# Performance work log

Hardware: AMD Instinct MI355X
Metric: run time of the kernel (lower is better)

Reference implementation:

```python
import jax, jax.numpy as jnp
import numpy as np

DT_RANK = 64
D_STATE = 16


def setup_inputs() -> dict:
    key = jax.random.key(0)
    ks = jax.random.split(key, 6)
    B, L, Di = 2, 2048, 2048
    x = jax.random.normal(ks[0], (B, L, Di), dtype=jnp.float32)
    W_xproj = jax.random.normal(ks[1], (DT_RANK + 2 * D_STATE, Di), dtype=jnp.float32) * (Di ** -0.5)
    W_dt = jax.random.uniform(ks[2], (Di, DT_RANK), dtype=jnp.float32, minval=-(DT_RANK ** -0.5), maxval=DT_RANK ** -0.5)
    dt = jnp.exp(jax.random.uniform(ks[3], (Di,), dtype=jnp.float32) * (np.log(0.1) - np.log(0.001)) + np.log(0.001))
    b_dt = dt + jnp.log(-jnp.expm1(-dt))
    A_log = jnp.log(jnp.broadcast_to(jnp.arange(1, D_STATE + 1, dtype=jnp.float32), (Di, D_STATE)))
    D_param = jnp.ones((Di,), dtype=jnp.float32)
    return {"x": x, "W_xproj": W_xproj, "W_dt": W_dt, "b_dt": b_dt, "A_log": A_log, "D_param": D_param}


def _selective_scan(u, delta, A, Bm, Cm):
    # u, delta: (b, l, d); A: (d, n); Bm, Cm: (b, l, n)
    deltaA = jnp.exp(delta[..., None] * A[None, None])          # (b, l, d, n)
    deltaB_u = delta[..., None] * Bm[:, :, None, :] * u[..., None]  # (b, l, d, n)

    def step(h, inp):
        dA, dBu, c = inp                      # dA,dBu: (b,d,n); c: (b,n)
        h = dA * h + dBu
        y = jnp.einsum('bdn,bn->bd', h, c)
        return h, y

    b, l, d = u.shape
    h0 = jnp.zeros((b, d, A.shape[1]), dtype=u.dtype)
    xs = (jnp.moveaxis(deltaA, 1, 0), jnp.moveaxis(deltaB_u, 1, 0), jnp.moveaxis(Cm, 1, 0))
    _, ys = jax.lax.scan(step, h0, xs)        # ys: (l, b, d)
    return jnp.moveaxis(ys, 0, 1)


def reference(x, W_xproj, W_dt, b_dt, A_log, D_param):
    x_dbl = jnp.einsum('bld,ed->ble', x, W_xproj)  # (b, l, dt_rank + 2*n)
    dlt = x_dbl[..., :DT_RANK]
    Bm = x_dbl[..., DT_RANK:DT_RANK + D_STATE]
    Cm = x_dbl[..., DT_RANK + D_STATE:]
    delta = jax.nn.softplus(jnp.einsum('blr,dr->bld', dlt, W_dt) + b_dt)
    A = -jnp.exp(A_log.astype(jnp.float32))
    y = _selective_scan(x, delta, A, Bm, Cm)
    return y + x * D_param[None, None, :]
```

## Files before the change

### kernel.cpp

```cpp
#include <hip/hip_runtime.h>

#define BATCH 2
#define L_SEQ 2048
#define DI 2048
#define NROW (BATCH * L_SEQ)
#define E_DIM 96
#define RNK 64
#define NST 16
#define NCH 64
#define CL 32
#define SPLITK 16
#define KSL (DI / SPLITK)

#define WS_XDBL 0
#define WS_PART 393216
#define WS_HLOC 393216
#define WS_DSUM (393216 + 4194304)
#define WS_HENT (393216 + 6291456)
#define WS_WDTT (393216 + 6291456)

__device__ __forceinline__ float softplusf(float z) {
    return fmaxf(z, 0.f) + __logf(1.f + __expf(-fabsf(z)));
}

__device__ __forceinline__ void barrier_lds() {
    asm volatile("s_waitcnt lgkmcnt(0)" ::: "memory");
    __builtin_amdgcn_s_barrier();
}

__global__ __launch_bounds__(256) void gemm_xproj_part(const float* __restrict__ x,
                                                       const float* __restrict__ Wx,
                                                       float* __restrict__ part) {
    __shared__ float xs[32][68];
    __shared__ float wsh[32][100];
    const int tid = threadIdx.x;
    const int r0 = blockIdx.x * 64;
    const int kbase0 = blockIdx.y * KSL;
    const int rg = tid >> 4;
    const int cg = tid & 15;

    float acc[4][6];
#pragma unroll
    for (int i = 0; i < 4; i++)
#pragma unroll
        for (int j = 0; j < 6; j++) acc[i][j] = 0.f;

    for (int kt = 0; kt < KSL / 32; kt++) {
        const int kb = kbase0 + kt * 32;
#pragma unroll
        for (int rep = 0; rep < 2; rep++) {
            int i = rep * 256 + tid;
            int row = i >> 3;
            int kq = i & 7;
            float4 v = *(const float4*)&x[(long)(r0 + row) * DI + kb + kq * 4];
            xs[kq * 4 + 0][row] = v.x;
            xs[kq * 4 + 1][row] = v.y;
            xs[kq * 4 + 2][row] = v.z;
            xs[kq * 4 + 3][row] = v.w;
        }
#pragma unroll
        for (int rep = 0; rep < 3; rep++) {
            int i = rep * 256 + tid;
            int e = i >> 3;
            int kq = i & 7;
            float4 v = *(const float4*)&Wx[(long)e * DI + kb + kq * 4];
            wsh[kq * 4 + 0][e] = v.x;
            wsh[kq * 4 + 1][e] = v.y;
            wsh[kq * 4 + 2][e] = v.z;
            wsh[kq * 4 + 3][e] = v.w;
        }
        __syncthreads();
#pragma unroll 8
        for (int k = 0; k < 32; k++) {
            float xr[4], wr[6];
#pragma unroll
            for (int i = 0; i < 4; i++) xr[i] = xs[k][rg * 4 + i];
#pragma unroll
            for (int j = 0; j < 6; j++) wr[j] = wsh[k][cg * 6 + j];
#pragma unroll
            for (int i = 0; i < 4; i++)
#pragma unroll
                for (int j = 0; j < 6; j++) acc[i][j] = fmaf(xr[i], wr[j], acc[i][j]);
        }
        __syncthreads();
    }
    const long sbase = (long)blockIdx.y * NROW * E_DIM;
#pragma unroll
    for (int i = 0; i < 4; i++) {
        long rowb = sbase + (long)(r0 + rg * 4 + i) * E_DIM + cg * 6;
#pragma unroll
        for (int j = 0; j < 6; j++) part[rowb + j] = acc[i][j];
    }
}

__global__ __launch_bounds__(256) void xproj_reduce_wt(const float* __restrict__ part,
                                                       float* __restrict__ xdbl,
                                                       const float* __restrict__ Wdt,
                                                       float* __restrict__ wdtT) {
    if (blockIdx.x < 384) {
        const int i4 = blockIdx.x * 256 + threadIdx.x;
        const float4* p4 = (const float4*)part;
        float4 s = p4[i4];
#pragma unroll
        for (int sp = 1; sp < SPLITK; sp++) {
            float4 v = p4[(long)sp * (NROW * E_DIM / 4) + i4];
            s.x += v.x; s.y += v.y; s.z += v.z; s.w += v.w;
        }
        ((float4*)xdbl)[i4] = s;
    } else {
        const int t = (blockIdx.x - 384) * 256 + threadIdx.x;
        const int base = t * 4;
        const int r = base >> 11;
        const int d4 = base & (DI - 1);
        float4 o;
        o.x = Wdt[(long)(d4 + 0) * RNK + r];
        o.y = Wdt[(long)(d4 + 1) * RNK + r];
        o.z = Wdt[(long)(d4 + 2) * RNK + r];
        o.w = Wdt[(long)(d4 + 3) * RNK + r];
        *(float4*)&wdtT[base] = o;
    }
}

#define PW 260
#define PD 36
__global__ __launch_bounds__(256) void gemm_dt_scan(const float* __restrict__ x,
                                                    const float* __restrict__ xdbl,
                                                    const float* __restrict__ wdtT,
                                                    const float* __restrict__ b_dt,
                                                    const float* __restrict__ A_log,
                                                    float* __restrict__ delta,
                                                    float* __restrict__ hloc,
                                                    float* __restrict__ dsumb) {
    __shared__ float region[32 * PW + 32 * PD];
    __shared__ float bsm[CL * NST];
    float* wt  = region;
    float* dlb = region + 32 * PW;
    float* dtt = region;

    const int tid = threadIdx.x;
    const int d0 = blockIdx.x * 256;
    const int c = blockIdx.y;
    const int b = blockIdx.z;
    const int row0 = b * L_SEQ + c * CL;
    const int d = d0 + tid;
    const int rg = tid >> 6;
    const int cg = tid & 63;

    if (tid < 128) {
        int r = tid >> 2, q = tid & 3;
        ((float4*)bsm)[tid] = *(const float4*)&xdbl[(long)(row0 + r) * E_DIM + 64 + q * 4];
    }

    float acc[8][4];
#pragma unroll
    for (int i = 0; i < 8; i++)
#pragma unroll
        for (int j = 0; j < 4; j++) acc[i][j] = 0.f;

    float xv[CL];
    float4 av[4];

#pragma unroll
    for (int kt = 0; kt < 2; kt++) {
        const int kb = kt * 32;
#pragma unroll
        for (int rep = 0; rep < 8; rep++) {
            int i = rep * 256 + tid;
            int k = i >> 6, c4 = i & 63;
            float4 v = *(const float4*)&wdtT[(long)(kb + k) * DI + d0 + c4 * 4];
            *(float4*)&wt[k * PW + c4 * 4] = v;
        }
        {
            int r = tid >> 3, kq = tid & 7;
            float4 v = *(const float4*)&xdbl[(long)(row0 + r) * E_DIM + kb + kq * 4];
            dlb[(kq * 4 + 0) * PD + r] = v.x;
            dlb[(kq * 4 + 1) * PD + r] = v.y;
            dlb[(kq * 4 + 2) * PD + r] = v.z;
            dlb[(kq * 4 + 3) * PD + r] = v.w;
        }
        if (kt == 0) {
#pragma unroll
            for (int ll = 0; ll < CL; ll++)
                xv[ll] = x[(long)(row0 + ll) * DI + d];
#pragma unroll
            for (int q = 0; q < 4; q++)
                av[q] = *(const float4*)&A_log[(long)d * NST + q * 4];
        }
        barrier_lds();
#pragma unroll 8
        for (int k = 0; k < 32; k++) {
            float4 xa = *(const float4*)&dlb[k * PD + rg * 8];
            float4 xb = *(const float4*)&dlb[k * PD + rg * 8 + 4];
            float4 wv4 = *(const float4*)&wt[k * PW + cg * 4];
            float xr[8] = {xa.x, xa.y, xa.z, xa.w, xb.x, xb.y, xb.z, xb.w};
            float wr[4] = {wv4.x, wv4.y, wv4.z, wv4.w};
#pragma unroll
            for (int i = 0; i < 8; i++)
#pragma unroll
                for (int j = 0; j < 4; j++) acc[i][j] = fmaf(xr[i], wr[j], acc[i][j]);
        }
        barrier_lds();
    }

    float4 bb = *(const float4*)&b_dt[d0 + cg * 4];
#pragma unroll
    for (int i = 0; i < 8; i++) {
        int r = rg * 8 + i;
        float4 o;
        o.x = softplusf(acc[i][0] + bb.x);
        o.y = softplusf(acc[i][1] + bb.y);
        o.z = softplusf(acc[i][2] + bb.z);
        o.w = softplusf(acc[i][3] + bb.w);
        *(float4*)&delta[(long)(row0 + r) * DI + d0 + cg * 4] = o;
        *(float4*)&dtt[r * 256 + cg * 4] = o;
    }

    float A[16];
#pragma unroll
    for (int q = 0; q < 4; q++) {
        A[q * 4 + 0] = -__expf(av[q].x);
        A[q * 4 + 1] = -__expf(av[q].y);
        A[q * 4 + 2] = -__expf(av[q].z);
        A[q * 4 + 3] = -__expf(av[q].w);
    }
    const float A0 = A[0];
    bool fast = true;
#pragma unroll
    for (int n = 1; n < 16; n++)
        fast = fast && (fabsf(A[n] - (float)(n + 1) * A0) <= 1e-4f * (float)(n + 1));
    barrier_lds();

    float h[16];
#pragma unroll
    for (int n = 0; n < 16; n++) h[n] = 0.f;
    float dsum = 0.f;
    if (fast) {
        for (int ll = 0; ll < CL; ll++) {
            float dc = dtt[ll * 256 + tid];
            float du = dc * xv[ll];
            float p1 = __expf(dc * A0);
            float p2 = p1 * p1, p3 = p2 * p1, p4 = p2 * p2, p5 = p3 * p2;
            float p6 = p3 * p3, p7 = p4 * p3, p8 = p4 * p4, p9 = p5 * p4;
            float p10 = p5 * p5, p11 = p6 * p5, p12 = p6 * p6, p13 = p7 * p6;
            float p14 = p7 * p7, p15 = p8 * p7, p16 = p8 * p8;
            float e_[16] = {p1, p2, p3, p4, p5, p6, p7, p8,
                            p9, p10, p11, p12, p13, p14, p15, p16};
#pragma unroll
            for (int q = 0; q < 4; q++) {
                float4 v = *(const float4*)&bsm[ll * NST + q * 4];
                h[q * 4 + 0] = fmaf(e_[q * 4 + 0], h[q * 4 + 0], du * v.x);
                h[q * 4 + 1] = fmaf(e_[q * 4 + 1], h[q * 4 + 1], du * v.y);
                h[q * 4 + 2] = fmaf(e_[q * 4 + 2], h[q * 4 + 2], du * v.z);
                h[q * 4 + 3] = fmaf(e_[q * 4 + 3], h[q * 4 + 3], du * v.w);
            }
            dsum += dc;
        }
    } else {
        for (int ll = 0; ll < CL; ll++) {
            float dc = dtt[ll * 256 + tid];
            float du = dc * xv[ll];
#pragma unroll
            for (int q = 0; q < 4; q++) {
                float4 v = *(const float4*)&bsm[ll * NST + q * 4];
                h[q * 4 + 0] = fmaf(__expf(dc * A[q * 4 + 0]), h[q * 4 + 0], du * v.x);
                h[q * 4 + 1] = fmaf(__expf(dc * A[q * 4 + 1]), h[q * 4 + 1], du * v.y);
                h[q * 4 + 2] = fmaf(__expf(dc * A[q * 4 + 2]), h[q * 4 + 2], du * v.z);
                h[q * 4 + 3] = fmaf(__expf(dc * A[q * 4 + 3]), h[q * 4 + 3], du * v.w);
            }
            dsum += dc;
        }
    }
    const long cb = (long)(b * NCH + c);
#pragma unroll
    for (int n = 0; n < 16; n++)
        hloc[(cb * NST + n) * DI + d] = h[n];
    dsumb[cb * DI + d] = dsum;
}

__global__ __launch_bounds__(256, 1) void scan_prefix(const float* __restrict__ A_log,
                                                      const float* __restrict__ hloc,
                                                      const float* __restrict__ dsumb,
                                                      float* __restrict__ hent) {
    const int g = blockIdx.x * 256 + threadIdx.x;
    const int d = g & (DI - 1);
    const int n = (g >> 11) & 15;
    const int b = g >> 15;
    const float An = -__expf(A_log[(long)d * NST + n]);
    float hl[NCH], dsv[NCH];
#pragma unroll
    for (int cc = 0; cc < NCH; cc++) {
        hl[cc]  = hloc[((long)(b * NCH + cc) * NST + n) * DI + d];
        dsv[cc] = dsumb[(long)(b * NCH + cc) * DI + d];
    }
    float e[NCH];
#pragma unroll
    for (int cc = 0; cc < NCH; cc++) e[cc] = __expf(An * dsv[cc]);
    float hc = 0.f;
#pragma unroll
    for (int cc = 0; cc < NCH; cc++) {
        hent[((long)(b * NCH + cc) * NST + n) * DI + d] = hc;
        hc = fmaf(e[cc], hc, hl[cc]);
    }
}

__global__ __launch_bounds__(256) void scan_out(const float* __restrict__ x,
                                                const float* __restrict__ xdbl,
                                                const float* __restrict__ A_log,
                                                const float* __restrict__ Dp,
                                                const float* __restrict__ hent,
                                                float* __restrict__ out) {
    __shared__ float bsm[CL * NST];
    __shared__ float csm[CL * NST];
    const int tid = threadIdx.x;
    const int d0 = blockIdx.x * 256;
    const int c = blockIdx.y;
    const int b = blockIdx.z;
    const int row0 = b * L_SEQ + c * CL;
    const int d = d0 + tid;

    {
        int i = tid & 127, r = i >> 2, q = i & 3;
        float4 v = *(const float4*)&xdbl[(long)(row0 + r) * E_DIM + 64 + ((tid >> 7) << 4) + q * 4];
        if (tid < 128) ((float4*)bsm)[i] = v;
        else           ((float4*)csm)[i] = v;
    }
    __syncthreads();

    float4 av[4];
#pragma unroll
    for (int q = 0; q < 4; q++)
        av[q] = *(const float4*)&A_log[(long)d * NST + q * 4];
    const long cb = (long)(b * NCH + c);
    float hv[16];
#pragma unroll
    for (int n = 0; n < 16; n++)
        hv[n] = hent[(cb * NST + n) * DI + d];
    const float Dd = Dp[d];

    float dv[CL], xv[CL];
#pragma unroll
    for (int ll = 0; ll < CL; ll++) {
        dv[ll] = out[(long)(row0 + ll) * DI + d];
        xv[ll] = x[(long)(row0 + ll) * DI + d];
    }

    float A[16];
#pragma unroll
    for (int q = 0; q < 4; q++) {
        A[q * 4 + 0] = -__expf(av[q].x);
        A[q * 4 + 1] = -__expf(av[q].y);
        A[q * 4 + 2] = -__expf(av[q].z);
        A[q * 4 + 3] = -__expf(av[q].w);
    }
    const float A0 = A[0];
    bool fast = true;
#pragma unroll
    for (int n = 1; n < 16; n++)
        fast = fast && (fabsf(A[n] - (float)(n + 1) * A0) <= 1e-4f * (float)(n + 1));
    float h[16];
#pragma unroll
    for (int n = 0; n < 16; n++) h[n] = hv[n];

    long idx = (long)row0 * DI + d;
    if (fast) {
        for (int ll = 0; ll < CL; ll++) {
            float dc = dv[ll];
            float xc = xv[ll];
            float du = dc * xc;
            float p1 = __expf(dc * A0);
            float p2 = p1 * p1, p3 = p2 * p1, p4 = p2 * p2, p5 = p3 * p2;
            float p6 = p3 * p3, p7 = p4 * p3, p8 = p4 * p4, p9 = p5 * p4;
            float p10 = p5 * p5, p11 = p6 * p5, p12 = p6 * p6, p13 = p7 * p6;
            float p14 = p7 * p7, p15 = p8 * p7, p16 = p8 * p8;
            float e_[16] = {p1, p2, p3, p4, p5, p6, p7, p8,
                            p9, p10, p11, p12, p13, p14, p15, p16};
            float y = 0.f;
#pragma unroll
            for (int q = 0; q < 4; q++) {
                float4 v = *(const float4*)&bsm[ll * NST + q * 4];
                float4 w = *(const float4*)&csm[ll * NST + q * 4];
                h[q * 4 + 0] = fmaf(e_[q * 4 + 0], h[q * 4 + 0], du * v.x);
                h[q * 4 + 1] = fmaf(e_[q * 4 + 1], h[q * 4 + 1], du * v.y);
                h[q * 4 + 2] = fmaf(e_[q * 4 + 2], h[q * 4 + 2], du * v.z);
                h[q * 4 + 3] = fmaf(e_[q * 4 + 3], h[q * 4 + 3], du * v.w);
                y = fmaf(h[q * 4 + 0], w.x, y);
                y = fmaf(h[q * 4 + 1], w.y, y);
                y = fmaf(h[q * 4 + 2], w.z, y);
                y = fmaf(h[q * 4 + 3], w.w, y);
            }
            out[idx] = fmaf(xc, Dd, y);
            idx += DI;
        }
    } else {
        for (int ll = 0; ll < CL; ll++) {
            float dc = dv[ll];
            float xc = xv[ll];
            float du = dc * xc;
            float y = 0.f;
#pragma unroll
            for (int q = 0; q < 4; q++) {
                float4 v = *(const float4*)&bsm[ll * NST + q * 4];
                float4 w = *(const float4*)&csm[ll * NST + q * 4];
                float e0 = __expf(dc * A[q * 4 + 0]);
                float e1 = __expf(dc * A[q * 4 + 1]);
                float e2 = __expf(dc * A[q * 4 + 2]);
                float e3 = __expf(dc * A[q * 4 + 3]);
                h[q * 4 + 0] = fmaf(e0, h[q * 4 + 0], du * v.x);
                h[q * 4 + 1] = fmaf(e1, h[q * 4 + 1], du * v.y);
                h[q * 4 + 2] = fmaf(e2, h[q * 4 + 2], du * v.z);
                h[q * 4 + 3] = fmaf(e3, h[q * 4 + 3], du * v.w);
                y = fmaf(h[q * 4 + 0], w.x, y);
                y = fmaf(h[q * 4 + 1], w.y, y);
                y = fmaf(h[q * 4 + 2], w.z, y);
                y = fmaf(h[q * 4 + 3], w.w, y);
            }
            out[idx] = fmaf(xc, Dd, y);
            idx += DI;
        }
    }
}

extern "C" void kernel_launch(void* const* d_in, const int* in_sizes, int n_in,
                              void* d_out, int out_size, void* d_ws, size_t ws_size,
                              hipStream_t stream) {
    const float* x    = (const float*)d_in[0];
    const float* Wx   = (const float*)d_in[1];
    const float* Wdt  = (const float*)d_in[2];
    const float* bdt  = (const float*)d_in[3];
    const float* Alog = (const float*)d_in[4];
    const float* Dp   = (const float*)d_in[5];
    float* out = (float*)d_out;
    float* ws = (float*)d_ws;
    float* xdbl  = ws + WS_XDBL;
    float* partb = ws + WS_PART;
    float* hloc  = ws + WS_HLOC;
    float* dsumb = ws + WS_DSUM;
    float* hent  = ws + WS_HENT;
    float* wdtT  = ws + WS_WDTT;

    gemm_xproj_part<<<dim3(NROW / 64, SPLITK), 256, 0, stream>>>(x, Wx, partb);
    xproj_reduce_wt<<<dim3(384 + 128), 256, 0, stream>>>(partb, xdbl, Wdt, wdtT);
    gemm_dt_scan<<<dim3(DI / 256, NCH, BATCH), 256, 0, stream>>>(x, xdbl, wdtT, bdt, Alog,
                                                                 out, hloc, dsumb);
    scan_prefix<<<dim3(BATCH * DI * NST / 256), 256, 0, stream>>>(Alog, hloc, dsumb, hent);
    scan_out<<<dim3(DI / 256, NCH, BATCH), 256, 0, stream>>>(x, xdbl, Alog, Dp, hent, out);
}
```

Before: 188.5 us.

## Fuse dt GEMM, chunk scan, prefix and output into one cooperative kernel

Replaces the three-kernel dt-GEMM/scan/prefix/output sequence with a single cooperative kernel that uses grid-wide syncs between the local chunk scan, the cross-chunk prefix and the output pass. Chunks grow to 64 steps, and delta, x, B and C stay in registers and LDS across phases. This removes the delta round trip through the output buffer, the x reload and two launches. In exchange it adds grid-sync cost, high register pressure from the 64-element per-thread arrays, and it only runs when occupancy allows all 512 blocks to be co-resident, otherwise falling back to the old kernels.

```diff
diff --git a/kernel.cpp b/kernel.cpp
--- a/kernel.cpp
+++ b/kernel.cpp
@@ -1,4 +1,6 @@
 #include <hip/hip_runtime.h>
+#include <hip/hip_cooperative_groups.h>
+namespace cg = cooperative_groups;
 
 #define BATCH 2
 #define L_SEQ 2048
@@ -7,6 +9,8 @@
 #define E_DIM 96
 #define RNK 64
 #define NST 16
+#define CLEN 64
+#define NCHG 32
 #define NCH 64
 #define CL 32
 #define SPLITK 16
@@ -14,10 +18,13 @@
 
 #define WS_XDBL 0
 #define WS_PART 393216
-#define WS_HLOC 393216
-#define WS_DSUM (393216 + 4194304)
-#define WS_HENT (393216 + 6291456)
-#define WS_WDTT (393216 + 6291456)
+#define WS_HLOC32 393216
+#define WS_DSUM32 2490368
+#define WS_HENT32 6684672
+#define WS_HLOC64 393216
+#define WS_DSUM64 4587520
+#define WS_HENT64 6684672
+#define WS_WDTT 8781824
 
 __device__ __forceinline__ float softplusf(float z) {
     return fmaxf(z, 0.f) + __logf(1.f + __expf(-fabsf(z)));
@@ -123,6 +130,287 @@
 
 #define PW 260
 #define PD 36
+#define PDF 68
+
+#define PCHAIN_E16(DCV) \
+    float p1 = __expf((DCV) * A0); \
+    float p2 = p1 * p1, p3 = p2 * p1, p4 = p2 * p2, p5 = p4 * p1; \
+    float p6 = p3 * p3, p7 = p4 * p3, p8 = p4 * p4; \
+    float e_[16] = {p1, p2, p3, p4, p5, p6, p7, p8, \
+                    p8 * p1, p5 * p5, p8 * p3, p6 * p6, \
+                    p8 * p5, p7 * p7, p8 * p7, p8 * p8};
+
+__global__ __launch_bounds__(256, 2) void ssm_fused(const float* __restrict__ x,
+                                                    const float* __restrict__ xdbl,
+                                                    const float* __restrict__ wdtT,
+                                                    const float* __restrict__ b_dt,
+                                                    const float* __restrict__ A_log,
+                                                    const float* __restrict__ Dp,
+                                                    float* __restrict__ hloc,
+                                                    float* __restrict__ dsumb,
+                                                    float* __restrict__ hent,
+                                                    float* __restrict__ out) {
+    __shared__ float region[16 * PW + 16 * PDF];
+    float* wt  = region;
+    float* dlb = region + 16 * PW;
+    float* dtt = region;
+    float* bsm = region;
+    float* csm = region + CLEN * NST;
+
+    const int tid = threadIdx.x;
+    const int bid = blockIdx.x;
+    const int d0 = (bid & 7) * 256;
+    const int c = (bid >> 3) & 31;
+    const int b = bid >> 8;
+    const int row0 = b * L_SEQ + c * CLEN;
+    const int d = d0 + tid;
+    const int rg = tid >> 6;
+    const int cg = tid & 63;
+
+    float4 wq[2][4]; float4 dq[2];
+#define ISSUE_Q(SET, Q) \
+    { _Pragma("unroll") \
+      for (int rep = 0; rep < 4; rep++) { \
+          int i = rep * 256 + tid; int kk = i >> 6, c4 = i & 63; \
+          wq[SET][rep] = *(const float4*)&wdtT[(long)((Q) * 16 + kk) * DI + d0 + c4 * 4]; } \
+      { int r = tid >> 2, kk = tid & 3; \
+        dq[SET] = *(const float4*)&xdbl[(long)(row0 + r) * E_DIM + (Q) * 16 + kk * 4]; } }
+#define WRITE_Q(SET) \
+    { _Pragma("unroll") \
+      for (int rep = 0; rep < 4; rep++) { \
+          int i = rep * 256 + tid; int kk = i >> 6, c4 = i & 63; \
+          *(float4*)&wt[kk * PW + c4 * 4] = wq[SET][rep]; } \
+      { int r = tid >> 2, kk = tid & 3; \
+        dlb[(kk * 4 + 0) * PDF + r] = dq[SET].x; \
+        dlb[(kk * 4 + 1) * PDF + r] = dq[SET].y; \
+        dlb[(kk * 4 + 2) * PDF + r] = dq[SET].z; \
+        dlb[(kk * 4 + 3) * PDF + r] = dq[SET].w; } }
+
+    ISSUE_Q(0, 0);
+    float4 av[4];
+#pragma unroll
+    for (int q = 0; q < 4; q++)
+        av[q] = *(const float4*)&A_log[(long)d * NST + q * 4];
+    float4 bb = *(const float4*)&b_dt[d0 + cg * 4];
+
+    WRITE_Q(0);
+    ISSUE_Q(1, 1);
+    barrier_lds();
+
+    float accA[8][4], accB[8][4];
+#pragma unroll
+    for (int i = 0; i < 8; i++)
+#pragma unroll
+        for (int j = 0; j < 4; j++) { accA[i][j] = 0.f; accB[i][j] = 0.f; }
+
+#pragma unroll
+    for (int qq = 0; qq < 4; qq++) {
+#pragma unroll
+        for (int k = 0; k < 16; k++) {
+            float4 a0 = *(const float4*)&dlb[k * PDF + rg * 8];
+            float4 a1 = *(const float4*)&dlb[k * PDF + rg * 8 + 4];
+            float4 b0 = *(const float4*)&dlb[k * PDF + 32 + rg * 8];
+            float4 b1 = *(const float4*)&dlb[k * PDF + 32 + rg * 8 + 4];
+            float4 w4 = *(const float4*)&wt[k * PW + cg * 4];
+            float ar[8] = {a0.x, a0.y, a0.z, a0.w, a1.x, a1.y, a1.z, a1.w};
+            float br[8] = {b0.x, b0.y, b0.z, b0.w, b1.x, b1.y, b1.z, b1.w};
+            float wr[4] = {w4.x, w4.y, w4.z, w4.w};
+#pragma unroll
+            for (int i = 0; i < 8; i++)
+#pragma unroll
+                for (int j = 0; j < 4; j++) {
+                    accA[i][j] = fmaf(ar[i], wr[j], accA[i][j]);
+                    accB[i][j] = fmaf(br[i], wr[j], accB[i][j]);
+                }
+        }
+        barrier_lds();
+        if (qq < 3) {
+            WRITE_Q((qq + 1) & 1);
+            if (qq < 2) ISSUE_Q(qq & 1, qq + 2);
+            barrier_lds();
+        }
+    }
+
+    float xv[CLEN];
+#pragma unroll
+    for (int ll = 0; ll < CLEN; ll++) xv[ll] = x[(long)(row0 + ll) * DI + d];
+
+    float A0; bool fast;
+    {
+        float a16[16];
+#pragma unroll
+        for (int q = 0; q < 4; q++) {
+            a16[q * 4 + 0] = -__expf(av[q].x);
+            a16[q * 4 + 1] = -__expf(av[q].y);
+            a16[q * 4 + 2] = -__expf(av[q].z);
+            a16[q * 4 + 3] = -__expf(av[q].w);
+        }
+        A0 = a16[0];
+        fast = true;
+#pragma unroll
+        for (int n = 1; n < 16; n++)
+            fast = fast && (fabsf(a16[n] - (float)(n + 1) * A0) <= 1e-4f * (float)(n + 1));
+    }
+
+    float dcl[CLEN];
+#define XROUND(ACC, RG0, TBASE) \
+    if (rg == (RG0) || rg == (RG0) + 1) { \
+        _Pragma("unroll") for (int i = 0; i < 8; i++) { \
+            float4 o; \
+            o.x = softplusf(ACC[i][0] + bb.x); \
+            o.y = softplusf(ACC[i][1] + bb.y); \
+            o.z = softplusf(ACC[i][2] + bb.z); \
+            o.w = softplusf(ACC[i][3] + bb.w); \
+            *(float4*)&dtt[((rg - (RG0)) * 8 + i) * 256 + cg * 4] = o; \
+        } \
+    } \
+    barrier_lds(); \
+    _Pragma("unroll") for (int ll = 0; ll < 16; ll++) dcl[(TBASE) + ll] = dtt[ll * 256 + tid]; \
+    barrier_lds();
+
+    XROUND(accA, 0, 0)
+    XROUND(accA, 2, 16)
+    XROUND(accB, 0, 32)
+    XROUND(accB, 2, 48)
+
+    { int r = tid >> 2, q = tid & 3;
+      float4 bv = *(const float4*)&xdbl[(long)(row0 + r) * E_DIM + 64 + q * 4];
+      float4 cv = *(const float4*)&xdbl[(long)(row0 + r) * E_DIM + 80 + q * 4];
+      *(float4*)&bsm[r * NST + q * 4] = bv;
+      *(float4*)&csm[r * NST + q * 4] = cv; }
+    barrier_lds();
+
+    float h[16];
+#pragma unroll
+    for (int n = 0; n < 16; n++) h[n] = 0.f;
+    float dsum = 0.f;
+    if (fast) {
+#pragma unroll
+        for (int ll = 0; ll < CLEN; ll++) {
+            float dcv = dcl[ll]; float du = dcv * xv[ll];
+            PCHAIN_E16(dcv);
+#pragma unroll
+            for (int q = 0; q < 4; q++) {
+                float4 v = *(const float4*)&bsm[ll * NST + q * 4];
+                h[q * 4 + 0] = fmaf(e_[q * 4 + 0], h[q * 4 + 0], du * v.x);
+                h[q * 4 + 1] = fmaf(e_[q * 4 + 1], h[q * 4 + 1], du * v.y);
+                h[q * 4 + 2] = fmaf(e_[q * 4 + 2], h[q * 4 + 2], du * v.z);
+                h[q * 4 + 3] = fmaf(e_[q * 4 + 3], h[q * 4 + 3], du * v.w);
+            }
+            dsum += dcv;
+        }
+    } else {
+        float Ag[16];
+#pragma unroll
+        for (int q = 0; q < 4; q++) {
+            Ag[q * 4 + 0] = -__expf(av[q].x); Ag[q * 4 + 1] = -__expf(av[q].y);
+            Ag[q * 4 + 2] = -__expf(av[q].z); Ag[q * 4 + 3] = -__expf(av[q].w);
+        }
+#pragma unroll
+        for (int ll = 0; ll < CLEN; ll++) {
+            float dcv = dcl[ll]; float du = dcv * xv[ll];
+#pragma unroll
+            for (int q = 0; q < 4; q++) {
+                float4 v = *(const float4*)&bsm[ll * NST + q * 4];
+                h[q * 4 + 0] = fmaf(__expf(dcv * Ag[q * 4 + 0]), h[q * 4 + 0], du * v.x);
+                h[q * 4 + 1] = fmaf(__expf(dcv * Ag[q * 4 + 1]), h[q * 4 + 1], du * v.y);
+                h[q * 4 + 2] = fmaf(__expf(dcv * Ag[q * 4 + 2]), h[q * 4 + 2], du * v.z);
+                h[q * 4 + 3] = fmaf(__expf(dcv * Ag[q * 4 + 3]), h[q * 4 + 3], du * v.w);
+            }
+            dsum += dcv;
+        }
+    }
+    const long cbq = (long)(b * NCHG + c);
+#pragma unroll
+    for (int n = 0; n < 16; n++)
+        hloc[(cbq * NST + n) * DI + d] = h[n];
+    dsumb[cbq * DI + d] = dsum;
+
+    __threadfence();
+    cg::this_grid().sync();
+
+    {
+        const int gi = bid * 256 + tid;
+        if (gi < BATCH * DI * NST) {
+            const int d2 = gi & (DI - 1);
+            const int n2 = (gi >> 11) & 15;
+            const int b2 = gi >> 15;
+            const float An = -__expf(A_log[(long)d2 * NST + n2]);
+            float hc = 0.f;
+#pragma unroll
+            for (int c8 = 0; c8 < NCHG; c8 += 8) {
+                float hl[8], ds8[8];
+#pragma unroll
+                for (int j = 0; j < 8; j++) {
+                    hl[j] = hloc[((long)(b2 * NCHG + c8 + j) * NST + n2) * DI + d2];
+                    ds8[j] = dsumb[(long)(b2 * NCHG + c8 + j) * DI + d2];
+                }
+#pragma unroll
+                for (int j = 0; j < 8; j++) {
+                    hent[((long)(b2 * NCHG + c8 + j) * NST + n2) * DI + d2] = hc;
+                    hc = fmaf(__expf(An * ds8[j]), hc, hl[j]);
+                }
+            }
+        }
+    }
+    __threadfence();
+    cg::this_grid().sync();
+
+    const float Dd = Dp[d];
+#pragma unroll
+    for (int n = 0; n < 16; n++)
+        h[n] = hent[(cbq * NST + n) * DI + d];
+
+    if (fast) {
+#pragma unroll
+        for (int ll = 0; ll < CLEN; ll++) {
+            float dcv = dcl[ll]; float xc = xv[ll]; float du = dcv * xc;
+            PCHAIN_E16(dcv);
+            float y = 0.f;
+#pragma unroll
+            for (int q = 0; q < 4; q++) {
+                float4 v = *(const float4*)&bsm[ll * NST + q * 4];
+                float4 w = *(const float4*)&csm[ll * NST + q * 4];
+                h[q * 4 + 0] = fmaf(e_[q * 4 + 0], h[q * 4 + 0], du * v.x);
+                h[q * 4 + 1] = fmaf(e_[q * 4 + 1], h[q * 4 + 1], du * v.y);
+                h[q * 4 + 2] = fmaf(e_[q * 4 + 2], h[q * 4 + 2], du * v.z);
+                h[q * 4 + 3] = fmaf(e_[q * 4 + 3], h[q * 4 + 3], du * v.w);
+                y = fmaf(h[q * 4 + 0], w.x, y);
+                y = fmaf(h[q * 4 + 1], w.y, y);
+                y = fmaf(h[q * 4 + 2], w.z, y);
+                y = fmaf(h[q * 4 + 3], w.w, y);
+            }
+            out[(long)(row0 + ll) * DI + d] = fmaf(xc, Dd, y);
+        }
+    } else {
+        float Ag[16];
+#pragma unroll
+        for (int q = 0; q < 4; q++) {
+            Ag[q * 4 + 0] = -__expf(av[q].x); Ag[q * 4 + 1] = -__expf(av[q].y);
+            Ag[q * 4 + 2] = -__expf(av[q].z); Ag[q * 4 + 3] = -__expf(av[q].w);
+        }
+#pragma unroll
+        for (int ll = 0; ll < CLEN; ll++) {
+            float dcv = dcl[ll]; float xc = xv[ll]; float du = dcv * xc;
+            float y = 0.f;
+#pragma unroll
+            for (int q = 0; q < 4; q++) {
+                float4 v = *(const float4*)&bsm[ll * NST + q * 4];
+                float4 w = *(const float4*)&csm[ll * NST + q * 4];
+                h[q * 4 + 0] = fmaf(__expf(dcv * Ag[q * 4 + 0]), h[q * 4 + 0], du * v.x);
+                h[q * 4 + 1] = fmaf(__expf(dcv * Ag[q * 4 + 1]), h[q * 4 + 1], du * v.y);
+                h[q * 4 + 2] = fmaf(__expf(dcv * Ag[q * 4 + 2]), h[q * 4 + 2], du * v.z);
+                h[q * 4 + 3] = fmaf(__expf(dcv * Ag[q * 4 + 3]), h[q * 4 + 3], du * v.w);
+                y = fmaf(h[q * 4 + 0], w.x, y);
+                y = fmaf(h[q * 4 + 1], w.y, y);
+                y = fmaf(h[q * 4 + 2], w.z, y);
+                y = fmaf(h[q * 4 + 3], w.w, y);
+            }
+            out[(long)(row0 + ll) * DI + d] = fmaf(xc, Dd, y);
+        }
+    }
+}
+
 __global__ __launch_bounds__(256) void gemm_dt_scan(const float* __restrict__ x,
                                                     const float* __restrict__ xdbl,
                                                     const float* __restrict__ wdtT,
@@ -157,7 +445,7 @@
 #pragma unroll
         for (int j = 0; j < 4; j++) acc[i][j] = 0.f;
 
-    float xv[CL];
+    float xvv[CL];
     float4 av[4];
 
 #pragma unroll
@@ -181,7 +469,7 @@
         if (kt == 0) {
 #pragma unroll
             for (int ll = 0; ll < CL; ll++)
-                xv[ll] = x[(long)(row0 + ll) * DI + d];
+                xvv[ll] = x[(long)(row0 + ll) * DI + d];
 #pragma unroll
             for (int q = 0; q < 4; q++)
                 av[q] = *(const float4*)&A_log[(long)d * NST + q * 4];
@@ -202,15 +490,15 @@
         barrier_lds();
     }
 
-    float4 bb = *(const float4*)&b_dt[d0 + cg * 4];
+    float4 bbf = *(const float4*)&b_dt[d0 + cg * 4];
 #pragma unroll
     for (int i = 0; i < 8; i++) {
         int r = rg * 8 + i;
         float4 o;
-        o.x = softplusf(acc[i][0] + bb.x);
-        o.y = softplusf(acc[i][1] + bb.y);
-        o.z = softplusf(acc[i][2] + bb.z);
-        o.w = softplusf(acc[i][3] + bb.w);
+        o.x = softplusf(acc[i][0] + bbf.x);
+        o.y = softplusf(acc[i][1] + bbf.y);
+        o.z = softplusf(acc[i][2] + bbf.z);
+        o.w = softplusf(acc[i][3] + bbf.w);
         *(float4*)&delta[(long)(row0 + r) * DI + d0 + cg * 4] = o;
         *(float4*)&dtt[r * 256 + cg * 4] = o;
     }
@@ -237,14 +525,8 @@
     if (fast) {
         for (int ll = 0; ll < CL; ll++) {
             float dc = dtt[ll * 256 + tid];
-            float du = dc * xv[ll];
-            float p1 = __expf(dc * A0);
-            float p2 = p1 * p1, p3 = p2 * p1, p4 = p2 * p2, p5 = p3 * p2;
-            float p6 = p3 * p3, p7 = p4 * p3, p8 = p4 * p4, p9 = p5 * p4;
-            float p10 = p5 * p5, p11 = p6 * p5, p12 = p6 * p6, p13 = p7 * p6;
-            float p14 = p7 * p7, p15 = p8 * p7, p16 = p8 * p8;
-            float e_[16] = {p1, p2, p3, p4, p5, p6, p7, p8,
-                            p9, p10, p11, p12, p13, p14, p15, p16};
+            float du = dc * xvv[ll];
+            PCHAIN_E16(dc);
 #pragma unroll
             for (int q = 0; q < 4; q++) {
                 float4 v = *(const float4*)&bsm[ll * NST + q * 4];
@@ -258,7 +540,7 @@
     } else {
         for (int ll = 0; ll < CL; ll++) {
             float dc = dtt[ll * 256 + tid];
-            float du = dc * xv[ll];
+            float du = dc * xvv[ll];
 #pragma unroll
             for (int q = 0; q < 4; q++) {
                 float4 v = *(const float4*)&bsm[ll * NST + q * 4];
@@ -337,11 +619,11 @@
         hv[n] = hent[(cb * NST + n) * DI + d];
     const float Dd = Dp[d];
 
-    float dv[CL], xv[CL];
+    float dv[CL], xvv[CL];
 #pragma unroll
     for (int ll = 0; ll < CL; ll++) {
         dv[ll] = out[(long)(row0 + ll) * DI + d];
-        xv[ll] = x[(long)(row0 + ll) * DI + d];
+        xvv[ll] = x[(long)(row0 + ll) * DI + d];
     }
 
     float A[16];
@@ -365,15 +647,9 @@
     if (fast) {
         for (int ll = 0; ll < CL; ll++) {
             float dc = dv[ll];
-            float xc = xv[ll];
+            float xc = xvv[ll];
             float du = dc * xc;
-            float p1 = __expf(dc * A0);
-            float p2 = p1 * p1, p3 = p2 * p1, p4 = p2 * p2, p5 = p3 * p2;
-            float p6 = p3 * p3, p7 = p4 * p3, p8 = p4 * p4, p9 = p5 * p4;
-            float p10 = p5 * p5, p11 = p6 * p5, p12 = p6 * p6, p13 = p7 * p6;
-            float p14 = p7 * p7, p15 = p8 * p7, p16 = p8 * p8;
-            float e_[16] = {p1, p2, p3, p4, p5, p6, p7, p8,
-                            p9, p10, p11, p12, p13, p14, p15, p16};
+            PCHAIN_E16(dc);
             float y = 0.f;
 #pragma unroll
             for (int q = 0; q < 4; q++) {
@@ -394,21 +670,17 @@
     } else {
         for (int ll = 0; ll < CL; ll++) {
             float dc = dv[ll];
-            float xc = xv[ll];
+            float xc = xvv[ll];
             float du = dc * xc;
             float y = 0.f;
 #pragma unroll
             for (int q = 0; q < 4; q++) {
                 float4 v = *(const float4*)&bsm[ll * NST + q * 4];
                 float4 w = *(const float4*)&csm[ll * NST + q * 4];
-                float e0 = __expf(dc * A[q * 4 + 0]);
-                float e1 = __expf(dc * A[q * 4 + 1]);
-                float e2 = __expf(dc * A[q * 4 + 2]);
-                float e3 = __expf(dc * A[q * 4 + 3]);
-                h[q * 4 + 0] = fmaf(e0, h[q * 4 + 0], du * v.x);
-                h[q * 4 + 1] = fmaf(e1, h[q * 4 + 1], du * v.y);
-                h[q * 4 + 2] = fmaf(e2, h[q * 4 + 2], du * v.z);
-                h[q * 4 + 3] = fmaf(e3, h[q * 4 + 3], du * v.w);
+                h[q * 4 + 0] = fmaf(__expf(dc * A[q * 4 + 0]), h[q * 4 + 0], du * v.x);
+                h[q * 4 + 1] = fmaf(__expf(dc * A[q * 4 + 1]), h[q * 4 + 1], du * v.y);
+                h[q * 4 + 2] = fmaf(__expf(dc * A[q * 4 + 2]), h[q * 4 + 2], du * v.z);
+                h[q * 4 + 3] = fmaf(__expf(dc * A[q * 4 + 3]), h[q * 4 + 3], du * v.w);
                 y = fmaf(h[q * 4 + 0], w.x, y);
                 y = fmaf(h[q * 4 + 1], w.y, y);
                 y = fmaf(h[q * 4 + 2], w.z, y);
@@ -431,17 +703,44 @@
     const float* Dp   = (const float*)d_in[5];
     float* out = (float*)d_out;
     float* ws = (float*)d_ws;
-    float* xdbl  = ws + WS_XDBL;
-    float* partb = ws + WS_PART;
-    float* hloc  = ws + WS_HLOC;
-    float* dsumb = ws + WS_DSUM;
-    float* hent  = ws + WS_HENT;
-    float* wdtT  = ws + WS_WDTT;
+    float* xdbl   = ws + WS_XDBL;
+    float* partb  = ws + WS_PART;
+    float* wdtT   = ws + WS_WDTT;
+    float* hloc32 = ws + WS_HLOC32;
+    float* dsum32 = ws + WS_DSUM32;
+    float* hent32 = ws + WS_HENT32;
+    float* hloc64 = ws + WS_HLOC64;
+    float* dsum64 = ws + WS_DSUM64;
+    float* hent64 = ws + WS_HENT64;
+
+    static int coop_ok = -1;
+    if (coop_ok < 0) {
+        int nb = 0, ncu = 0, dev = 0;
+        (void)hipGetDevice(&dev);
+        hipError_t e1 = hipOccupancyMaxActiveBlocksPerMultiprocessor(
+            &nb, (const void*)ssm_fused, 256, 0);
+        hipError_t e2 = hipDeviceGetAttribute(
+            &ncu, hipDeviceAttributeMultiprocessorCount, dev);
+        coop_ok = (e1 == hipSuccess && e2 == hipSuccess &&
+                   (long)nb * ncu >= BATCH * NCHG * 8) ? 1 : 0;
+    }
 
     gemm_xproj_part<<<dim3(NROW / 64, SPLITK), 256, 0, stream>>>(x, Wx, partb);
-    xproj_reduce_wt<<<dim3(384 + 128), 256, 0, stream>>>(partb, xdbl, Wdt, wdtT);
-    gemm_dt_scan<<<dim3(DI / 256, NCH, BATCH), 256, 0, stream>>>(x, xdbl, wdtT, bdt, Alog,
-                                                                 out, hloc, dsumb);
-    scan_prefix<<<dim3(BATCH * DI * NST / 256), 256, 0, stream>>>(Alog, hloc, dsumb, hent);
-    scan_out<<<dim3(DI / 256, NCH, BATCH), 256, 0, stream>>>(x, xdbl, Alog, Dp, hent, out);
-}
+    xproj_reduce_wt<<<dim3(512), 256, 0, stream>>>(partb, xdbl, Wdt, wdtT);
+
+    bool done = false;
+    if (coop_ok == 1) {
+        void* args[] = {(void*)&x, (void*)&xdbl, (void*)&wdtT, (void*)&bdt, (void*)&Alog,
+                        (void*)&Dp, (void*)&hloc32, (void*)&dsum32, (void*)&hent32, (void*)&out};
+        hipError_t le = hipLaunchCooperativeKernel((const void*)ssm_fused,
+                                                   dim3(BATCH * NCHG * 8), dim3(256),
+                                                   args, 0, stream);
+        done = (le == hipSuccess);
+    }
+    if (!done) {
+        gemm_dt_scan<<<dim3(DI / 256, NCH, BATCH), 256, 0, stream>>>(x, xdbl, wdtT, bdt, Alog,
+                                                                     out, hloc64, dsum64);
+        scan_prefix<<<dim3(BATCH * DI * NST / 256), 256, 0, stream>>>(Alog, hloc64, dsum64, hent64);
+        scan_out<<<dim3(DI / 256, NCH, BATCH), 256, 0, stream>>>(x, xdbl, Alog, Dp, hent64, out);
+    }
+}
```

After: 192.7 us. +2.3%, slower.

## Use 512-thread blocks, split scan state across thread halves, stream W_dt tiles

Applied to the files above, without the earlier changes.

gemm_xproj_part now uses 512-thread blocks covering 128 rows, with vectorized LDS reads of the x tile. gemm_dt_scan moves to 512 threads: the dt GEMM stages W_dt in four 16-row rounds to cut LDS use, and the local chunk scan splits the 16 state lanes into two halves of 8 per thread. x loads are double-buffered across 8-step batches, and the power chain becomes incremental multiplies. The aim is more parallelism and lower register and LDS pressure per thread, in exchange for more barriers, a reworked delta staging order, and a longer multiply chain in the fast path.

```diff
diff --git a/kernel.cpp b/kernel.cpp
--- a/kernel.cpp
+++ b/kernel.cpp
@@ -28,13 +28,13 @@
     __builtin_amdgcn_s_barrier();
 }
 
-__global__ __launch_bounds__(256) void gemm_xproj_part(const float* __restrict__ x,
+__global__ __launch_bounds__(512) void gemm_xproj_part(const float* __restrict__ x,
                                                        const float* __restrict__ Wx,
                                                        float* __restrict__ part) {
-    __shared__ float xs[32][68];
+    __shared__ float xs[32][132];
     __shared__ float wsh[32][100];
     const int tid = threadIdx.x;
-    const int r0 = blockIdx.x * 64;
+    const int r0 = blockIdx.x * 128;
     const int kbase0 = blockIdx.y * KSL;
     const int rg = tid >> 4;
     const int cg = tid & 15;
@@ -49,32 +49,37 @@
         const int kb = kbase0 + kt * 32;
 #pragma unroll
         for (int rep = 0; rep < 2; rep++) {
-            int i = rep * 256 + tid;
-            int row = i >> 3;
-            int kq = i & 7;
+            int i = rep * 512 + tid;
+            int row = i >> 3, kq = i & 7;
             float4 v = *(const float4*)&x[(long)(r0 + row) * DI + kb + kq * 4];
             xs[kq * 4 + 0][row] = v.x;
             xs[kq * 4 + 1][row] = v.y;
             xs[kq * 4 + 2][row] = v.z;
             xs[kq * 4 + 3][row] = v.w;
         }
-#pragma unroll
-        for (int rep = 0; rep < 3; rep++) {
-            int i = rep * 256 + tid;
-            int e = i >> 3;
-            int kq = i & 7;
+        {
+            int e = tid >> 3, kq = tid & 7;
             float4 v = *(const float4*)&Wx[(long)e * DI + kb + kq * 4];
             wsh[kq * 4 + 0][e] = v.x;
             wsh[kq * 4 + 1][e] = v.y;
             wsh[kq * 4 + 2][e] = v.z;
             wsh[kq * 4 + 3][e] = v.w;
         }
+        if (tid < 256) {
+            int i = 512 + tid;
+            int e = i >> 3, kq = i & 7;
+            float4 v = *(const float4*)&Wx[(long)e * DI + kb + kq * 4];
+            wsh[kq * 4 + 0][e] = v.x;
+            wsh[kq * 4 + 1][e] = v.y;
+            wsh[kq * 4 + 2][e] = v.z;
+            wsh[kq * 4 + 3][e] = v.w;
+        }
         __syncthreads();
 #pragma unroll 8
         for (int k = 0; k < 32; k++) {
-            float xr[4], wr[6];
-#pragma unroll
-            for (int i = 0; i < 4; i++) xr[i] = xs[k][rg * 4 + i];
+            float4 xa = *(const float4*)&xs[k][rg * 4];
+            float xr[4] = {xa.x, xa.y, xa.z, xa.w};
+            float wr[6];
 #pragma unroll
             for (int j = 0; j < 6; j++) wr[j] = wsh[k][cg * 6 + j];
 #pragma unroll
@@ -121,20 +126,20 @@
     }
 }
 
-#define PW 260
-#define PD 36
-__global__ __launch_bounds__(256) void gemm_dt_scan(const float* __restrict__ x,
-                                                    const float* __restrict__ xdbl,
-                                                    const float* __restrict__ wdtT,
-                                                    const float* __restrict__ b_dt,
-                                                    const float* __restrict__ A_log,
-                                                    float* __restrict__ delta,
-                                                    float* __restrict__ hloc,
-                                                    float* __restrict__ dsumb) {
-    __shared__ float region[32 * PW + 32 * PD];
+#define PWT 256
+#define PDC 36
+__global__ __launch_bounds__(512, 6) void gemm_dt_scan(const float* __restrict__ x,
+                                                       const float* __restrict__ xdbl,
+                                                       const float* __restrict__ wdtT,
+                                                       const float* __restrict__ b_dt,
+                                                       const float* __restrict__ A_log,
+                                                       float* __restrict__ delta,
+                                                       float* __restrict__ hloc,
+                                                       float* __restrict__ dsumb) {
+    __shared__ float region[16 * PWT + RNK * PDC];
     __shared__ float bsm[CL * NST];
     float* wt  = region;
-    float* dlb = region + 32 * PW;
+    float* dlb = region + 16 * PWT;
     float* dtt = region;
 
     const int tid = threadIdx.x;
@@ -142,149 +147,198 @@
     const int c = blockIdx.y;
     const int b = blockIdx.z;
     const int row0 = b * L_SEQ + c * CL;
-    const int d = d0 + tid;
+    const int dcol = tid & 255;
+    const int d = d0 + dcol;
+    const int half = tid >> 8;
     const int rg = tid >> 6;
     const int cg = tid & 63;
 
+#define STAGE_WT(RND) { \
+    _Pragma("unroll") \
+    for (int rep = 0; rep < 2; rep++) { \
+        int i = rep * 512 + tid; int k = i >> 6, c4 = i & 63; \
+        *(float4*)&wt[k * PWT + c4 * 4] = \
+            *(const float4*)&wdtT[(long)((RND) * 16 + k) * DI + d0 + c4 * 4]; } }
+
+    STAGE_WT(0);
+    {
+        int r = tid >> 4, kq = tid & 15;
+        float4 v = *(const float4*)&xdbl[(long)(row0 + r) * E_DIM + kq * 4];
+        dlb[(kq * 4 + 0) * PDC + r] = v.x;
+        dlb[(kq * 4 + 1) * PDC + r] = v.y;
+        dlb[(kq * 4 + 2) * PDC + r] = v.z;
+        dlb[(kq * 4 + 3) * PDC + r] = v.w;
+    }
     if (tid < 128) {
         int r = tid >> 2, q = tid & 3;
         ((float4*)bsm)[tid] = *(const float4*)&xdbl[(long)(row0 + r) * E_DIM + 64 + q * 4];
     }
-
-    float acc[8][4];
-#pragma unroll
-    for (int i = 0; i < 8; i++)
+    float4 av0 = *(const float4*)&A_log[(long)d * NST + 0];
+    float4 av1 = *(const float4*)&A_log[(long)d * NST + 4];
+    float4 av2 = *(const float4*)&A_log[(long)d * NST + 8];
+    float4 av3 = *(const float4*)&A_log[(long)d * NST + 12];
+    float4 bb  = *(const float4*)&b_dt[d0 + cg * 4];
+
+    float acc[4][4];
+#pragma unroll
+    for (int i = 0; i < 4; i++)
 #pragma unroll
         for (int j = 0; j < 4; j++) acc[i][j] = 0.f;
 
-    float xv[CL];
-    float4 av[4];
-
-#pragma unroll
-    for (int kt = 0; kt < 2; kt++) {
-        const int kb = kt * 32;
-#pragma unroll
-        for (int rep = 0; rep < 8; rep++) {
-            int i = rep * 256 + tid;
-            int k = i >> 6, c4 = i & 63;
-            float4 v = *(const float4*)&wdtT[(long)(kb + k) * DI + d0 + c4 * 4];
-            *(float4*)&wt[k * PW + c4 * 4] = v;
-        }
-        {
-            int r = tid >> 3, kq = tid & 7;
-            float4 v = *(const float4*)&xdbl[(long)(row0 + r) * E_DIM + kb + kq * 4];
-            dlb[(kq * 4 + 0) * PD + r] = v.x;
-            dlb[(kq * 4 + 1) * PD + r] = v.y;
-            dlb[(kq * 4 + 2) * PD + r] = v.z;
-            dlb[(kq * 4 + 3) * PD + r] = v.w;
-        }
-        if (kt == 0) {
-#pragma unroll
-            for (int ll = 0; ll < CL; ll++)
-                xv[ll] = x[(long)(row0 + ll) * DI + d];
-#pragma unroll
-            for (int q = 0; q < 4; q++)
-                av[q] = *(const float4*)&A_log[(long)d * NST + q * 4];
+    barrier_lds();
+#pragma unroll
+    for (int rnd = 0; rnd < 4; rnd++) {
+#pragma unroll 8
+        for (int k = 0; k < 16; k++) {
+            float4 xa = *(const float4*)&dlb[(rnd * 16 + k) * PDC + rg * 4];
+            float4 w4 = *(const float4*)&wt[k * PWT + cg * 4];
+            float xr[4] = {xa.x, xa.y, xa.z, xa.w};
+#pragma unroll
+            for (int i = 0; i < 4; i++) {
+                acc[i][0] = fmaf(xr[i], w4.x, acc[i][0]);
+                acc[i][1] = fmaf(xr[i], w4.y, acc[i][1]);
+                acc[i][2] = fmaf(xr[i], w4.z, acc[i][2]);
+                acc[i][3] = fmaf(xr[i], w4.w, acc[i][3]);
+            }
         }
         barrier_lds();
-#pragma unroll 8
-        for (int k = 0; k < 32; k++) {
-            float4 xa = *(const float4*)&dlb[k * PD + rg * 8];
-            float4 xb = *(const float4*)&dlb[k * PD + rg * 8 + 4];
-            float4 wv4 = *(const float4*)&wt[k * PW + cg * 4];
-            float xr[8] = {xa.x, xa.y, xa.z, xa.w, xb.x, xb.y, xb.z, xb.w};
-            float wr[4] = {wv4.x, wv4.y, wv4.z, wv4.w};
-#pragma unroll
-            for (int i = 0; i < 8; i++)
-#pragma unroll
-                for (int j = 0; j < 4; j++) acc[i][j] = fmaf(xr[i], wr[j], acc[i][j]);
-        }
-        barrier_lds();
-    }
-
-    float4 bb = *(const float4*)&b_dt[d0 + cg * 4];
-#pragma unroll
-    for (int i = 0; i < 8; i++) {
-        int r = rg * 8 + i;
-        float4 o;
-        o.x = softplusf(acc[i][0] + bb.x);
-        o.y = softplusf(acc[i][1] + bb.y);
-        o.z = softplusf(acc[i][2] + bb.z);
-        o.w = softplusf(acc[i][3] + bb.w);
-        *(float4*)&delta[(long)(row0 + r) * DI + d0 + cg * 4] = o;
-        *(float4*)&dtt[r * 256 + cg * 4] = o;
-    }
-
-    float A[16];
-#pragma unroll
-    for (int q = 0; q < 4; q++) {
-        A[q * 4 + 0] = -__expf(av[q].x);
-        A[q * 4 + 1] = -__expf(av[q].y);
-        A[q * 4 + 2] = -__expf(av[q].z);
-        A[q * 4 + 3] = -__expf(av[q].w);
-    }
-    const float A0 = A[0];
+        if (rnd < 3) {
+            STAGE_WT(rnd + 1);
+            barrier_lds();
+        }
+    }
+
+#pragma unroll
+    for (int i = 0; i < 4; i++) {
+        acc[i][0] = softplusf(acc[i][0] + bb.x);
+        acc[i][1] = softplusf(acc[i][1] + bb.y);
+        acc[i][2] = softplusf(acc[i][2] + bb.z);
+        acc[i][3] = softplusf(acc[i][3] + bb.w);
+        float4 o = {acc[i][0], acc[i][1], acc[i][2], acc[i][3]};
+        *(float4*)&delta[(long)(row0 + rg * 4 + i) * DI + d0 + cg * 4] = o;
+    }
+
+    float a16[16];
+    a16[0] = -__expf(av0.x); a16[1] = -__expf(av0.y);
+    a16[2] = -__expf(av0.z); a16[3] = -__expf(av0.w);
+    a16[4] = -__expf(av1.x); a16[5] = -__expf(av1.y);
+    a16[6] = -__expf(av1.z); a16[7] = -__expf(av1.w);
+    a16[8] = -__expf(av2.x); a16[9] = -__expf(av2.y);
+    a16[10] = -__expf(av2.z); a16[11] = -__expf(av2.w);
+    a16[12] = -__expf(av3.x); a16[13] = -__expf(av3.y);
+    a16[14] = -__expf(av3.z); a16[15] = -__expf(av3.w);
+    const float A0 = a16[0];
     bool fast = true;
 #pragma unroll
     for (int n = 1; n < 16; n++)
-        fast = fast && (fabsf(A[n] - (float)(n + 1) * A0) <= 1e-4f * (float)(n + 1));
+        fast = fast && (fabsf(a16[n] - (float)(n + 1) * A0) <= 1e-4f * (float)(n + 1));
+    const float A0f = A0 * (float)(8 * half + 1);
+    float g[8];
+#pragma unroll
+    for (int j = 0; j < 8; j++) g[j] = half ? a16[8 + j] : a16[j];
+
+#define LOADX(XA, LL0) { _Pragma("unroll") \
+    for (int j = 0; j < 8; j++) XA[j] = x[(long)(row0 + (LL0) + j) * DI + d]; }
+#define COPYX { _Pragma("unroll") for (int j = 0; j < 8; j++) xcur[j] = xnxt[j]; }
+
+#define SCAN_BATCH(LL0, SL0, XA) \
+    if (fast) { \
+        _Pragma("unroll") \
+        for (int j = 0; j < 8; j++) { \
+            float dc = dtt[((SL0) + j) * 256 + dcol]; \
+            float du = dc * XA[j]; \
+            float4 v0 = *(const float4*)&bsm[((LL0) + j) * NST + half * 8]; \
+            float4 v1 = *(const float4*)&bsm[((LL0) + j) * NST + half * 8 + 4]; \
+            float p1 = __expf(dc * A0); \
+            float e  = __expf(dc * A0f); \
+            h[0] = fmaf(e, h[0], du * v0.x); e *= p1; \
+            h[1] = fmaf(e, h[1], du * v0.y); e *= p1; \
+            h[2] = fmaf(e, h[2], du * v0.z); e *= p1; \
+            h[3] = fmaf(e, h[3], du * v0.w); e *= p1; \
+            h[4] = fmaf(e, h[4], du * v1.x); e *= p1; \
+            h[5] = fmaf(e, h[5], du * v1.y); e *= p1; \
+            h[6] = fmaf(e, h[6], du * v1.z); e *= p1; \
+            h[7] = fmaf(e, h[7], du * v1.w); \
+            dsum += dc; \
+        } \
+    } else { \
+        _Pragma("unroll") \
+        for (int j = 0; j < 8; j++) { \
+            float dc = dtt[((SL0) + j) * 256 + dcol]; \
+            float du = dc * XA[j]; \
+            float4 v0 = *(const float4*)&bsm[((LL0) + j) * NST + half * 8]; \
+            float4 v1 = *(const float4*)&bsm[((LL0) + j) * NST + half * 8 + 4]; \
+            h[0] = fmaf(__expf(dc * g[0]), h[0], du * v0.x); \
+            h[1] = fmaf(__expf(dc * g[1]), h[1], du * v0.y); \
+            h[2] = fmaf(__expf(dc * g[2]), h[2], du * v0.z); \
+            h[3] = fmaf(__expf(dc * g[3]), h[3], du * v0.w); \
+            h[4] = fmaf(__expf(dc * g[4]), h[4], du * v1.x); \
+            h[5] = fmaf(__expf(dc * g[5]), h[5], du * v1.y); \
+            h[6] = fmaf(__expf(dc * g[6]), h[6], du * v1.z); \
+            h[7] = fmaf(__expf(dc * g[7]), h[7], du * v1.w); \
+            dsum += dc; \
+        } \
+    }
+
+    float xcur[8], xnxt[8];
+    LOADX(xcur, 0);
+    if (rg < 4) {
+#pragma unroll
+        for (int i = 0; i < 4; i++) {
+            float4 o = {acc[i][0], acc[i][1], acc[i][2], acc[i][3]};
+            *(float4*)&dtt[(rg * 4 + i) * 256 + cg * 4] = o;
+        }
+    }
     barrier_lds();
 
-    float h[16];
-#pragma unroll
-    for (int n = 0; n < 16; n++) h[n] = 0.f;
+    float h[8];
+#pragma unroll
+    for (int j = 0; j < 8; j++) h[j] = 0.f;
     float dsum = 0.f;
-    if (fast) {
-        for (int ll = 0; ll < CL; ll++) {
-            float dc = dtt[ll * 256 + tid];
-            float du = dc * xv[ll];
-            float p1 = __expf(dc * A0);
-            float p2 = p1 * p1, p3 = p2 * p1, p4 = p2 * p2, p5 = p3 * p2;
-            float p6 = p3 * p3, p7 = p4 * p3, p8 = p4 * p4, p9 = p5 * p4;
-            float p10 = p5 * p5, p11 = p6 * p5, p12 = p6 * p6, p13 = p7 * p6;
-            float p14 = p7 * p7, p15 = p8 * p7, p16 = p8 * p8;
-            float e_[16] = {p1, p2, p3, p4, p5, p6, p7, p8,
-                            p9, p10, p11, p12, p13, p14, p15, p16};
-#pragma unroll
-            for (int q = 0; q < 4; q++) {
-                float4 v = *(const float4*)&bsm[ll * NST + q * 4];
-                h[q * 4 + 0] = fmaf(e_[q * 4 + 0], h[q * 4 + 0], du * v.x);
-                h[q * 4 + 1] = fmaf(e_[q * 4 + 1], h[q * 4 + 1], du * v.y);
-                h[q * 4 + 2] = fmaf(e_[q * 4 + 2], h[q * 4 + 2], du * v.z);
-                h[q * 4 + 3] = fmaf(e_[q * 4 + 3], h[q * 4 + 3], du * v.w);
-            }
-            dsum += dc;
-        }
-    } else {
-        for (int ll = 0; ll < CL; ll++) {
-            float dc = dtt[ll * 256 + tid];
-            float du = dc * xv[ll];
-#pragma unroll
-            for (int q = 0; q < 4; q++) {
-                float4 v = *(const float4*)&bsm[ll * NST + q * 4];
-                h[q * 4 + 0] = fmaf(__expf(dc * A[q * 4 + 0]), h[q * 4 + 0], du * v.x);
-                h[q * 4 + 1] = fmaf(__expf(dc * A[q * 4 + 1]), h[q * 4 + 1], du * v.y);
-                h[q * 4 + 2] = fmaf(__expf(dc * A[q * 4 + 2]), h[q * 4 + 2], du * v.z);
-                h[q * 4 + 3] = fmaf(__expf(dc * A[q * 4 + 3]), h[q * 4 + 3], du * v.w);
-            }
-            dsum += dc;
-        }
-    }
+
+    LOADX(xnxt, 8);
+    SCAN_BATCH(0, 0, xcur);
+    COPYX;
+    LOADX(xnxt, 16);
+    SCAN_BATCH(8, 8, xcur);
+    COPYX;
+    barrier_lds();
+    if (rg >= 4) {
+#pragma unroll
+        for (int i = 0; i < 4; i++) {
+            float4 o = {acc[i][0], acc[i][1], acc[i][2], acc[i][3]};
+            *(float4*)&dtt[((rg - 4) * 4 + i) * 256 + cg * 4] = o;
+        }
+    }
+    barrier_lds();
+    LOADX(xnxt, 24);
+    SCAN_BATCH(16, 0, xcur);
+    COPYX;
+    SCAN_BATCH(24, 8, xcur);
+
     const long cb = (long)(b * NCH + c);
 #pragma unroll
-    for (int n = 0; n < 16; n++)
-        hloc[(cb * NST + n) * DI + d] = h[n];
-    dsumb[cb * DI + d] = dsum;
-}
+    for (int j = 0; j < 8; j++)
+        hloc[(cb * NST + half * 8 + j) * DI + d] = h[j];
+    if (half == 0) dsumb[cb * DI + d] = dsum;
+}
+
+#define PCHAIN_E16(DCV) \
+    float p1 = __expf((DCV) * A0); \
+    float p2 = p1 * p1, p3 = p2 * p1, p4 = p2 * p2, p5 = p4 * p1; \
+    float p6 = p3 * p3, p7 = p4 * p3, p8 = p4 * p4; \
+    float e_[16] = {p1, p2, p3, p4, p5, p6, p7, p8, \
+                    p8 * p1, p5 * p5, p8 * p3, p6 * p6, \
+                    p8 * p5, p7 * p7, p8 * p7, p8 * p8};
 
 __global__ __launch_bounds__(256, 1) void scan_prefix(const float* __restrict__ A_log,
                                                       const float* __restrict__ hloc,
                                                       const float* __restrict__ dsumb,
                                                       float* __restrict__ hent) {
-    const int g = blockIdx.x * 256 + threadIdx.x;
-    const int d = g & (DI - 1);
-    const int n = (g >> 11) & 15;
-    const int b = g >> 15;
+    const int gidx = blockIdx.x * 256 + threadIdx.x;
+    const int d = gidx & (DI - 1);
+    const int n = (gidx >> 11) & 15;
+    const int b = gidx >> 15;
     const float An = -__expf(A_log[(long)d * NST + n]);
     float hl[NCH], dsv[NCH];
 #pragma unroll
@@ -337,11 +391,11 @@
         hv[n] = hent[(cb * NST + n) * DI + d];
     const float Dd = Dp[d];
 
-    float dv[CL], xv[CL];
+    float dv[CL], xvv[CL];
 #pragma unroll
     for (int ll = 0; ll < CL; ll++) {
         dv[ll] = out[(long)(row0 + ll) * DI + d];
-        xv[ll] = x[(long)(row0 + ll) * DI + d];
+        xvv[ll] = x[(long)(row0 + ll) * DI + d];
     }
 
     float A[16];
@@ -365,15 +419,9 @@
     if (fast) {
         for (int ll = 0; ll < CL; ll++) {
             float dc = dv[ll];
-            float xc = xv[ll];
+            float xc = xvv[ll];
             float du = dc * xc;
-            float p1 = __expf(dc * A0);
-            float p2 = p1 * p1, p3 = p2 * p1, p4 = p2 * p2, p5 = p3 * p2;
-            float p6 = p3 * p3, p7 = p4 * p3, p8 = p4 * p4, p9 = p5 * p4;
-            float p10 = p5 * p5, p11 = p6 * p5, p12 = p6 * p6, p13 = p7 * p6;
-            float p14 = p7 * p7, p15 = p8 * p7, p16 = p8 * p8;
-            float e_[16] = {p1, p2, p3, p4, p5, p6, p7, p8,
-                            p9, p10, p11, p12, p13, p14, p15, p16};
+            PCHAIN_E16(dc);
             float y = 0.f;
 #pragma unroll
             for (int q = 0; q < 4; q++) {
@@ -394,21 +442,17 @@
     } else {
         for (int ll = 0; ll < CL; ll++) {
             float dc = dv[ll];
-            float xc = xv[ll];
+            float xc = xvv[ll];
             float du = dc * xc;
             float y = 0.f;
 #pragma unroll
             for (int q = 0; q < 4; q++) {
                 float4 v = *(const float4*)&bsm[ll * NST + q * 4];
                 float4 w = *(const float4*)&csm[ll * NST + q * 4];
-                float e0 = __expf(dc * A[q * 4 + 0]);
-                float e1 = __expf(dc * A[q * 4 + 1]);
-                float e2 = __expf(dc * A[q * 4 + 2]);
-                float e3 = __expf(dc * A[q * 4 + 3]);
-                h[q * 4 + 0] = fmaf(e0, h[q * 4 + 0], du * v.x);
-                h[q * 4 + 1] = fmaf(e1, h[q * 4 + 1], du * v.y);
-                h[q * 4 + 2] = fmaf(e2, h[q * 4 + 2], du * v.z);
-                h[q * 4 + 3] = fmaf(e3, h[q * 4 + 3], du * v.w);
+                h[q * 4 + 0] = fmaf(__expf(dc * A[q * 4 + 0]), h[q * 4 + 0], du * v.x);
+                h[q * 4 + 1] = fmaf(__expf(dc * A[q * 4 + 1]), h[q * 4 + 1], du * v.y);
+                h[q * 4 + 2] = fmaf(__expf(dc * A[q * 4 + 2]), h[q * 4 + 2], du * v.z);
+                h[q * 4 + 3] = fmaf(__expf(dc * A[q * 4 + 3]), h[q * 4 + 3], du * v.w);
                 y = fmaf(h[q * 4 + 0], w.x, y);
                 y = fmaf(h[q * 4 + 1], w.y, y);
                 y = fmaf(h[q * 4 + 2], w.z, y);
@@ -438,9 +482,9 @@
     float* hent  = ws + WS_HENT;
     float* wdtT  = ws + WS_WDTT;
 
-    gemm_xproj_part<<<dim3(NROW / 64, SPLITK), 256, 0, stream>>>(x, Wx, partb);
-    xproj_reduce_wt<<<dim3(384 + 128), 256, 0, stream>>>(partb, xdbl, Wdt, wdtT);
-    gemm_dt_scan<<<dim3(DI / 256, NCH, BATCH), 256, 0, stream>>>(x, xdbl, wdtT, bdt, Alog,
+    gemm_xproj_part<<<dim3(NROW / 128, SPLITK), 512, 0, stream>>>(x, Wx, partb);
+    xproj_reduce_wt<<<dim3(512), 256, 0, stream>>>(partb, xdbl, Wdt, wdtT);
+    gemm_dt_scan<<<dim3(DI / 256, NCH, BATCH), 512, 0, stream>>>(x, xdbl, wdtT, bdt, Alog,
                                                                  out, hloc, dsumb);
     scan_prefix<<<dim3(BATCH * DI * NST / 256), 256, 0, stream>>>(Alog, hloc, dsumb, hent);
     scan_out<<<dim3(DI / 256, NCH, BATCH), 256, 0, stream>>>(x, xdbl, Alog, Dp, hent, out);
```

New measurement: 215.6 us. 14.4% more time.
